# Performance work log

Hardware: AMD Instinct MI355X
Metric: run time of the kernel (lower is better)

Reference implementation:

```python
import jax, jax.numpy as jnp
import numpy as np

E, T, D_IN, D_H = 8, 4096, 2048, 1408

def setup_inputs() -> dict:
    key = jax.random.key(0)
    k_x, k_g, k_d, k_u = jax.random.split(key, 4)
    x = jax.random.normal(k_x, (E, T, D_IN), dtype=jnp.float32)
    gate_proj = jax.random.normal(k_g, (E, D_IN, D_H), dtype=jnp.float32) * 0.02
    down_proj = jax.random.normal(k_d, (E, D_IN, D_H), dtype=jnp.float32) * 0.02
    up_proj = jax.random.normal(k_u, (E, D_H, D_IN), dtype=jnp.float32) * 0.02
    return {"x": x, "gate_proj": gate_proj, "down_proj": down_proj,
            "up_proj": up_proj, "tokens_per_expert": T}

def reference(x, gate_proj, down_proj, up_proj, tokens_per_expert):
    # ep_size == 1 -> dispatch/combine are identity; x: [E, T, dim_in]
    # SwiGLU: h = silu(x @ gate) * (x @ down); out = h @ up
    h = jax.nn.silu(jnp.einsum('etd,edh->eth', x, gate_proj)) \
        * jnp.einsum('etd,edh->eth', x, down_proj)
    out = jnp.einsum('eth,ehd->etd', h, up_proj)
    return out
```

## Files before the change

### kernel.cpp

```cpp
#include <hip/hip_runtime.h>
#include <hip/hip_bf16.h>


typedef __bf16 bf16x8 __attribute__((ext_vector_type(8)));
typedef float  f32x4  __attribute__((ext_vector_type(4)));

__device__ __forceinline__ void gload16(const void* g, void* l) {
  __builtin_amdgcn_global_load_lds((const __attribute__((address_space(1))) void*)g,
                                   (__attribute__((address_space(3))) void*)l,
                                   16, 0, 0);
}

__device__ __forceinline__ unsigned short f2bf(float f) {
  union { float fv; unsigned u; } v; v.fv = f;
  unsigned r = (v.u + 0x7fffu + ((v.u >> 16) & 1u)) >> 16;
  return (unsigned short)r;
}

__global__ __launch_bounds__(256)
void cvt_f32_bf16(const float* __restrict__ in, unsigned short* __restrict__ out,
                  long n) {
  long i = ((long)blockIdx.x * 256 + threadIdx.x) * 4;
  const long stride = (long)gridDim.x * 1024;
  for (; i < n; i += stride) {
    const float4 v = *(const float4*)(in + i);
    ushort4 o;
    o.x = f2bf(v.x); o.y = f2bf(v.y); o.z = f2bf(v.z); o.w = f2bf(v.w);
    *(ushort4*)(out + i) = o;
  }
}

__global__ __launch_bounds__(256)
void trcvt(const float* __restrict__ in, unsigned short* __restrict__ out,
           int R, int C) {
  __shared__ unsigned short tile[32][33];
  const float* src = in + (size_t)blockIdx.z * R * C;
  unsigned short* dst = out + (size_t)blockIdx.z * R * C;
  const int c0 = blockIdx.x << 5, r0 = blockIdx.y << 5;
  const int tx = threadIdx.x, ty = threadIdx.y;
#pragma unroll
  for (int i = 0; i < 32; i += 8)
    tile[ty + i][tx] = f2bf(src[(size_t)(r0 + ty + i) * C + (c0 + tx)]);
  __syncthreads();
#pragma unroll
  for (int i = 0; i < 32; i += 8)
    dst[(size_t)(c0 + ty + i) * R + (r0 + tx)] = tile[tx][ty + i];
}

template <int KDIM, int NDIM, bool FUSED, bool F32OUT, int MINW>
__global__ __launch_bounds__(256, MINW)
void gemm_bt(const unsigned short* __restrict__ A,
             const unsigned short* __restrict__ B0,
             const unsigned short* __restrict__ B1,
             void* __restrict__ Cout) {
  __shared__ __align__(16) unsigned short sA[128 * 32];
  __shared__ __align__(16) unsigned short sB0[128 * 32];
  __shared__ __align__(16) unsigned short sB1[FUSED ? 128 * 32 : 8];

  const int t = threadIdx.x;
  const int w = t >> 6;
  const int lane = t & 63;
  const int e = blockIdx.z;
  const int m0 = blockIdx.y << 7;
  const int n0 = blockIdx.x << 7;

  const unsigned short* Ae  = A  + (size_t)e * 4096 * KDIM;
  const unsigned short* B0e = B0 + (size_t)e * NDIM * KDIM;
  const unsigned short* B1e = nullptr;
  if (FUSED) B1e = B1 + (size_t)e * NDIM * KDIM;

  const int srow  = lane >> 2;
  const int selem = ((lane & 3) ^ ((lane >> 3) & 3)) * 8;
  const unsigned short* aSrc[2];
  const unsigned short* b0Src[2];
  const unsigned short* b1Src[2];
  unsigned short *aDst[2], *b0Dst[2], *b1Dst[2];
#pragma unroll
  for (int i = 0; i < 2; ++i) {
    const int c = 2 * w + i;
    aSrc[i]  = Ae  + (size_t)(m0 + c * 16 + srow) * KDIM + selem;
    b0Src[i] = B0e + (size_t)(n0 + c * 16 + srow) * KDIM + selem;
    aDst[i]  = &sA[c * 512];
    b0Dst[i] = &sB0[c * 512];
    if (FUSED) {
      b1Src[i] = B1e + (size_t)(n0 + c * 16 + srow) * KDIM + selem;
      b1Dst[i] = &sB1[c * 512];
    }
  }

  f32x4 acc0[4][4], acc1[4][4];
  const f32x4 z = {0.f, 0.f, 0.f, 0.f};
#pragma unroll
  for (int mi = 0; mi < 4; ++mi)
#pragma unroll
    for (int ni = 0; ni < 4; ++ni) { acc0[mi][ni] = z; acc1[mi][ni] = z; }

  const bf16x8* pA  = (const bf16x8*)sA;
  const bf16x8* pB0 = (const bf16x8*)sB0;
  const bf16x8* pB1 = (const bf16x8*)sB1;
  const int wm = (w >> 1) << 6;
  const int wn = (w & 1) << 6;
  const int lm = lane & 15;
  const int kq = lane >> 4;
  const int ksw = kq ^ ((lm >> 1) & 3);
  const int fa = (wm + lm) * 4 + ksw;
  const int fb = (wn + lm) * 4 + ksw;

  for (int kk = 0; kk < KDIM / 32; ++kk) {
    __syncthreads();
#pragma unroll
    for (int i = 0; i < 2; ++i) {
      gload16(aSrc[i],  aDst[i]);   aSrc[i]  += 32;
      gload16(b0Src[i], b0Dst[i]);  b0Src[i] += 32;
      if (FUSED) { gload16(b1Src[i], b1Dst[i]); b1Src[i] += 32; }
    }
    __syncthreads();

    bf16x8 af[4], bf0[4], bf1[4];
#pragma unroll
    for (int mi = 0; mi < 4; ++mi) af[mi] = pA[fa + (mi << 6)];
#pragma unroll
    for (int ni = 0; ni < 4; ++ni) {
      bf0[ni] = pB0[fb + (ni << 6)];
      if (FUSED) bf1[ni] = pB1[fb + (ni << 6)];
    }
#pragma unroll
    for (int mi = 0; mi < 4; ++mi)
#pragma unroll
      for (int ni = 0; ni < 4; ++ni) {
        acc0[mi][ni] = __builtin_amdgcn_mfma_f32_16x16x32_bf16(af[mi], bf0[ni], acc0[mi][ni], 0, 0, 0);
        if (FUSED)
          acc1[mi][ni] = __builtin_amdgcn_mfma_f32_16x16x32_bf16(af[mi], bf1[ni], acc1[mi][ni], 0, 0, 0);
      }
  }

#pragma unroll
  for (int mi = 0; mi < 4; ++mi)
#pragma unroll
    for (int ni = 0; ni < 4; ++ni)
#pragma unroll
      for (int i = 0; i < 4; ++i) {
        const int row = m0 + wm + (mi << 4) + (kq << 2) + i;
        const int col = n0 + wn + (ni << 4) + lm;
        float v = acc0[mi][ni][i];
        if (FUSED) {
          const float g = v;
          const float d = acc1[mi][ni][i];
          v = g / (1.0f + __expf(-g)) * d;
        }
        const size_t idx = (size_t)e * 4096 * NDIM + (size_t)row * NDIM + col;
        if (F32OUT) ((float*)Cout)[idx] = v;
        else        ((unsigned short*)Cout)[idx] = f2bf(v);
      }
}

extern "C" void kernel_launch(void* const* d_in, const int* in_sizes, int n_in,
                              void* d_out, int out_size, void* d_ws, size_t ws_size,
                              hipStream_t stream) {
  const float* x    = (const float*)d_in[0];
  const float* gate = (const float*)d_in[1];
  const float* down = (const float*)d_in[2];
  const float* up   = (const float*)d_in[3];

  unsigned short* xb = (unsigned short*)d_out;

  char* ws = (char*)d_ws;
  unsigned short* h    = (unsigned short*)ws;
  unsigned short* bufG = (unsigned short*)(ws + 92274688ull);
  unsigned short* bufD = (unsigned short*)(ws + 138412032ull);

  const long nx = 8L * 4096 * 2048;
  cvt_f32_bf16<<<8192, 256, 0, stream>>>(x, xb, nx);

  dim3 tb(32, 8, 1);
  trcvt<<<dim3(44, 64, 8), tb, 0, stream>>>(gate, bufG, 2048, 1408);
  trcvt<<<dim3(44, 64, 8), tb, 0, stream>>>(down, bufD, 2048, 1408);
  gemm_bt<2048, 1408, true, false, 2><<<dim3(11, 32, 8), 256, 0, stream>>>(xb, bufG, bufD, h);
  trcvt<<<dim3(64, 44, 8), tb, 0, stream>>>(up, bufG, 1408, 2048);
  gemm_bt<1408, 2048, false, true, 3><<<dim3(16, 32, 8), 256, 0, stream>>>(h, bufG, nullptr, (float*)d_out);
}
```

Measured before the change: 1.284 ms.

## Rewrite GEMMs as 8-wave double-buffered kernels with larger tiles and XCD swizzle

After: 1.459 ms. 13.7% more time.

```diff
diff --git a/kernel.cpp b/kernel.cpp
--- a/kernel.cpp
+++ b/kernel.cpp
@@ -47,111 +47,184 @@
     dst[(size_t)(c0 + ty + i) * R + (r0 + tx)] = tile[tx][ty + i];
 }
 
-template <int KDIM, int NDIM, bool FUSED, bool F32OUT, int MINW>
-__global__ __launch_bounds__(256, MINW)
-void gemm_bt(const unsigned short* __restrict__ A,
-             const unsigned short* __restrict__ B0,
-             const unsigned short* __restrict__ B1,
-             void* __restrict__ Cout) {
-  __shared__ __align__(16) unsigned short sA[128 * 32];
-  __shared__ __align__(16) unsigned short sB0[128 * 32];
-  __shared__ __align__(16) unsigned short sB1[FUSED ? 128 * 32 : 8];
+template <int KDIM, int NDIM, bool FUSED, bool F32OUT>
+__global__ __launch_bounds__(512, 2)
+void gemm8p(const unsigned short* __restrict__ A,
+            const unsigned short* __restrict__ B0,
+            const unsigned short* __restrict__ B1,
+            void* __restrict__ Cout) {
+  constexpr int BM  = 256;
+  constexpr int BN  = FUSED ? 128 : 256;
+  constexpr int NB_N = NDIM / BN;
+  constexpr int NKT = KDIM / 64;
+  constexpr int PMI = FUSED ? 2 : 4;
+  constexpr int NMI = FUSED ? 4 : 8;
+
+  __shared__ __align__(16) unsigned short sA[2][BM * 64];
+  __shared__ __align__(16) unsigned short sB[2][(FUSED ? 2 : 1) * BN * 64];
 
   const int t = threadIdx.x;
   const int w = t >> 6;
   const int lane = t & 63;
-  const int e = blockIdx.z;
-  const int m0 = blockIdx.y << 7;
-  const int n0 = blockIdx.x << 7;
+  const int e = blockIdx.y;
+
+  const int cpx = gridDim.x >> 3;
+  const int bid = (blockIdx.x & 7) * cpx + (blockIdx.x >> 3);
+  const int m0 = (bid / NB_N) << 8;
+  const int n0 = (bid % NB_N) * BN;
 
   const unsigned short* Ae  = A  + (size_t)e * 4096 * KDIM;
   const unsigned short* B0e = B0 + (size_t)e * NDIM * KDIM;
-  const unsigned short* B1e = nullptr;
-  if (FUSED) B1e = B1 + (size_t)e * NDIM * KDIM;
-
-  const int srow  = lane >> 2;
-  const int selem = ((lane & 3) ^ ((lane >> 3) & 3)) * 8;
-  const unsigned short* aSrc[2];
-  const unsigned short* b0Src[2];
-  const unsigned short* b1Src[2];
-  unsigned short *aDst[2], *b0Dst[2], *b1Dst[2];
-#pragma unroll
-  for (int i = 0; i < 2; ++i) {
-    const int c = 2 * w + i;
-    aSrc[i]  = Ae  + (size_t)(m0 + c * 16 + srow) * KDIM + selem;
-    b0Src[i] = B0e + (size_t)(n0 + c * 16 + srow) * KDIM + selem;
-    aDst[i]  = &sA[c * 512];
-    b0Dst[i] = &sB0[c * 512];
-    if (FUSED) {
-      b1Src[i] = B1e + (size_t)(n0 + c * 16 + srow) * KDIM + selem;
-      b1Dst[i] = &sB1[c * 512];
+
+  const int l8 = lane >> 3;
+  const int lc = ((lane & 7) ^ l8) << 3;
+
+  const unsigned short* aSrc[4];
+  const unsigned short* bSrc[4];
+#pragma unroll
+  for (int i = 0; i < 4; ++i)
+    aSrc[i] = Ae + (size_t)(m0 + ((4 * w + i) << 3) + l8) * KDIM + lc;
+  if constexpr (FUSED) {
+    const unsigned short* B1e = B1 + (size_t)e * NDIM * KDIM;
+#pragma unroll
+    for (int j = 0; j < 2; ++j) {
+      bSrc[j]     = B0e + (size_t)(n0 + ((2 * w + j) << 3) + l8) * KDIM + lc;
+      bSrc[2 + j] = B1e + (size_t)(n0 + ((2 * w + j) << 3) + l8) * KDIM + lc;
     }
-  }
-
-  f32x4 acc0[4][4], acc1[4][4];
-  const f32x4 z = {0.f, 0.f, 0.f, 0.f};
-#pragma unroll
-  for (int mi = 0; mi < 4; ++mi)
-#pragma unroll
-    for (int ni = 0; ni < 4; ++ni) { acc0[mi][ni] = z; acc1[mi][ni] = z; }
-
-  const bf16x8* pA  = (const bf16x8*)sA;
-  const bf16x8* pB0 = (const bf16x8*)sB0;
-  const bf16x8* pB1 = (const bf16x8*)sB1;
-  const int wm = (w >> 1) << 6;
-  const int wn = (w & 1) << 6;
+  } else {
+#pragma unroll
+    for (int i = 0; i < 4; ++i)
+      bSrc[i] = B0e + (size_t)(n0 + ((4 * w + i) << 3) + l8) * KDIM + lc;
+  }
+
+  auto stage = [&](int nb) {
+#pragma unroll
+    for (int i = 0; i < 4; ++i) {
+      gload16(aSrc[i], &sA[nb][(4 * w + i) << 9]);
+      aSrc[i] += 64;
+    }
+    if constexpr (FUSED) {
+#pragma unroll
+      for (int j = 0; j < 2; ++j) {
+        gload16(bSrc[j], &sB[nb][(2 * w + j) << 9]);
+        bSrc[j] += 64;
+        gload16(bSrc[2 + j], &sB[nb][(BN * 64) + ((2 * w + j) << 9)]);
+        bSrc[2 + j] += 64;
+      }
+    } else {
+#pragma unroll
+      for (int i = 0; i < 4; ++i) {
+        gload16(bSrc[i], &sB[nb][(4 * w + i) << 9]);
+        bSrc[i] += 64;
+      }
+    }
+  };
+
+  const int wm = FUSED ? ((w >> 1) << 6) : ((w >> 2) << 7);
+  const int wn = FUSED ? ((w & 1) << 6) : ((w & 3) << 6);
   const int lm = lane & 15;
   const int kq = lane >> 4;
-  const int ksw = kq ^ ((lm >> 1) & 3);
-  const int fa = (wm + lm) * 4 + ksw;
-  const int fb = (wn + lm) * 4 + ksw;
-
-  for (int kk = 0; kk < KDIM / 32; ++kk) {
-    __syncthreads();
-#pragma unroll
-    for (int i = 0; i < 2; ++i) {
-      gload16(aSrc[i],  aDst[i]);   aSrc[i]  += 32;
-      gload16(b0Src[i], b0Dst[i]);  b0Src[i] += 32;
-      if (FUSED) { gload16(b1Src[i], b1Dst[i]); b1Src[i] += 32; }
-    }
-    __syncthreads();
-
-    bf16x8 af[4], bf0[4], bf1[4];
-#pragma unroll
-    for (int mi = 0; mi < 4; ++mi) af[mi] = pA[fa + (mi << 6)];
-#pragma unroll
-    for (int ni = 0; ni < 4; ++ni) {
-      bf0[ni] = pB0[fb + (ni << 6)];
-      if (FUSED) bf1[ni] = pB1[fb + (ni << 6)];
-    }
+
+  f32x4 acc0[NMI][4];
+  f32x4 acc1[FUSED ? 4 : 1][4];
+  const f32x4 z = {0.f, 0.f, 0.f, 0.f};
+#pragma unroll
+  for (int mi = 0; mi < NMI; ++mi)
+#pragma unroll
+    for (int ni = 0; ni < 4; ++ni) acc0[mi][ni] = z;
+  if constexpr (FUSED) {
 #pragma unroll
     for (int mi = 0; mi < 4; ++mi)
 #pragma unroll
-      for (int ni = 0; ni < 4; ++ni) {
-        acc0[mi][ni] = __builtin_amdgcn_mfma_f32_16x16x32_bf16(af[mi], bf0[ni], acc0[mi][ni], 0, 0, 0);
-        if (FUSED)
-          acc1[mi][ni] = __builtin_amdgcn_mfma_f32_16x16x32_bf16(af[mi], bf1[ni], acc1[mi][ni], 0, 0, 0);
-      }
-  }
-
-#pragma unroll
-  for (int mi = 0; mi < 4; ++mi)
-#pragma unroll
-    for (int ni = 0; ni < 4; ++ni)
-#pragma unroll
-      for (int i = 0; i < 4; ++i) {
-        const int row = m0 + wm + (mi << 4) + (kq << 2) + i;
-        const int col = n0 + wn + (ni << 4) + lm;
-        float v = acc0[mi][ni][i];
-        if (FUSED) {
-          const float g = v;
+      for (int ni = 0; ni < 4; ++ni) acc1[mi][ni] = z;
+  }
+
+  bf16x8 af[PMI][2], bf0[2][2], bf1[2][2];
+
+  auto ldf = [&](const unsigned short* base, int rowbase, int ks) -> bf16x8 {
+    const int r = rowbase + lm;
+    const int c = ((ks << 2) + kq) ^ (lm & 7);
+    return ((const bf16x8*)base)[(r << 3) + c];
+  };
+
+#define PHASE(bufA, bufB, ABLK, BPAIR, READA, TILEEND)                         \
+  {                                                                            \
+    if constexpr (READA) {                                                     \
+      _Pragma("unroll") for (int mi = 0; mi < PMI; ++mi)                       \
+        _Pragma("unroll") for (int ks = 0; ks < 2; ++ks)                       \
+          af[mi][ks] = ldf(bufA, wm + (((ABLK)*PMI + mi) << 4), ks);           \
+    }                                                                          \
+    _Pragma("unroll") for (int nj = 0; nj < 2; ++nj)                           \
+      _Pragma("unroll") for (int ks = 0; ks < 2; ++ks) {                       \
+        bf0[nj][ks] = ldf(bufB, wn + (((BPAIR)*2 + nj) << 4), ks);             \
+        if constexpr (FUSED)                                                   \
+          bf1[nj][ks] = ldf((bufB) + BN * 64, wn + (((BPAIR)*2 + nj) << 4), ks); \
+      }                                                                        \
+    __builtin_amdgcn_s_barrier();                                              \
+    asm volatile("s_waitcnt lgkmcnt(0)" ::: "memory");                         \
+    __builtin_amdgcn_s_setprio(1);                                             \
+    _Pragma("unroll") for (int mi = 0; mi < PMI; ++mi)                         \
+      _Pragma("unroll") for (int nj = 0; nj < 2; ++nj)                         \
+        _Pragma("unroll") for (int ks = 0; ks < 2; ++ks) {                     \
+          acc0[(ABLK)*PMI + mi][(BPAIR)*2 + nj] =                              \
+              __builtin_amdgcn_mfma_f32_16x16x32_bf16(                         \
+                  af[mi][ks], bf0[nj][ks],                                     \
+                  acc0[(ABLK)*PMI + mi][(BPAIR)*2 + nj], 0, 0, 0);             \
+          if constexpr (FUSED)                                                 \
+            acc1[(ABLK)*PMI + mi][(BPAIR)*2 + nj] =                            \
+                __builtin_amdgcn_mfma_f32_16x16x32_bf16(                       \
+                    af[mi][ks], bf1[nj][ks],                                   \
+                    acc1[(ABLK)*PMI + mi][(BPAIR)*2 + nj], 0, 0, 0);           \
+        }                                                                      \
+    __builtin_amdgcn_s_setprio(0);                                             \
+    if constexpr (TILEEND) asm volatile("s_waitcnt vmcnt(0)" ::: "memory");    \
+    __builtin_amdgcn_s_barrier();                                              \
+  }
+
+  stage(0);
+  asm volatile("s_waitcnt vmcnt(0)" ::: "memory");
+  __builtin_amdgcn_s_barrier();
+
+  for (int kt = 0; kt < NKT; ++kt) {
+    const int cur = kt & 1;
+    const unsigned short* bufA = sA[cur];
+    const unsigned short* bufB = sB[cur];
+    if (kt + 1 < NKT) stage(cur ^ 1);
+    PHASE(bufA, bufB, 0, 0, true,  false)
+    PHASE(bufA, bufB, 0, 1, false, false)
+    PHASE(bufA, bufB, 1, 0, true,  false)
+    PHASE(bufA, bufB, 1, 1, false, true)
+  }
+#undef PHASE
+
+  const size_t cbase = (size_t)e * 4096 * NDIM;
+  if constexpr (F32OUT) {
+    float* C = (float*)Cout + cbase;
+#pragma unroll
+    for (int mi = 0; mi < NMI; ++mi)
+#pragma unroll
+      for (int ni = 0; ni < 4; ++ni)
+#pragma unroll
+        for (int i = 0; i < 4; ++i) {
+          const int row = m0 + wm + (mi << 4) + (kq << 2) + i;
+          const int col = n0 + wn + (ni << 4) + lm;
+          C[(size_t)row * NDIM + col] = acc0[mi][ni][i];
+        }
+  } else {
+    unsigned short* C = (unsigned short*)Cout + cbase;
+#pragma unroll
+    for (int mi = 0; mi < NMI; ++mi)
+#pragma unroll
+      for (int ni = 0; ni < 4; ++ni)
+#pragma unroll
+        for (int i = 0; i < 4; ++i) {
+          const int row = m0 + wm + (mi << 4) + (kq << 2) + i;
+          const int col = n0 + wn + (ni << 4) + lm;
+          const float g = acc0[mi][ni][i];
           const float d = acc1[mi][ni][i];
-          v = g / (1.0f + __expf(-g)) * d;
+          C[(size_t)row * NDIM + col] = f2bf(g / (1.0f + __expf(-g)) * d);
         }
-        const size_t idx = (size_t)e * 4096 * NDIM + (size_t)row * NDIM + col;
-        if (F32OUT) ((float*)Cout)[idx] = v;
-        else        ((unsigned short*)Cout)[idx] = f2bf(v);
-      }
+  }
 }
 
 extern "C" void kernel_launch(void* const* d_in, const int* in_sizes, int n_in,
@@ -175,7 +248,10 @@
   dim3 tb(32, 8, 1);
   trcvt<<<dim3(44, 64, 8), tb, 0, stream>>>(gate, bufG, 2048, 1408);
   trcvt<<<dim3(44, 64, 8), tb, 0, stream>>>(down, bufD, 2048, 1408);
-  gemm_bt<2048, 1408, true, false, 2><<<dim3(11, 32, 8), 256, 0, stream>>>(xb, bufG, bufD, h);
+
+  gemm8p<2048, 1408, true, false><<<dim3(176, 8), 512, 0, stream>>>(xb, bufG, bufD, h);
+
   trcvt<<<dim3(64, 44, 8), tb, 0, stream>>>(up, bufG, 1408, 2048);
-  gemm_bt<1408, 2048, false, true, 3><<<dim3(16, 32, 8), 256, 0, stream>>>(h, bufG, nullptr, (float*)d_out);
-}
+
+  gemm8p<1408, 2048, false, true><<<dim3(128, 8), 512, 0, stream>>>(h, bufG, nullptr, (float*)d_out);
+}
```
